# Optimization experiments

Hardware: AMD Instinct MI355X
Metric: run time of the kernel (lower is better)

The kernel has to match this reference:

```python
import jax, jax.numpy as jnp
import numpy as np

N_NODES = 60000
SEQ_LEN = 30
VOCAB = 50000
D_IN = 100     # text_input_size
H = 100        # tweet_embed_size (GRU hidden)
H1 = 100       # hidden_size1
H2 = 100       # hidden_size2
N_EDGES = 120000
N_BATCH = 128


def setup_inputs() -> dict:
    key = jax.random.key(0)
    ks = jax.random.split(key, 16)
    s = 0.05
    return {
        'merged_tree_feature': jax.random.randint(ks[0], (N_NODES, SEQ_LEN), 0, VOCAB, dtype=jnp.int64) if jax.config.jax_enable_x64 else jax.random.randint(ks[0], (N_NODES, SEQ_LEN), 0, VOCAB, dtype=jnp.int32),
        'merged_tree_edge_index': jax.random.randint(ks[1], (2, N_EDGES), 0, N_NODES, dtype=jnp.int32),
        'indices': jax.random.randint(ks[2], (N_NODES,), 0, N_BATCH, dtype=jnp.int32),
        'h0': jax.random.normal(ks[3], (1, N_NODES, H), dtype=jnp.float32),
        'emb': jax.random.normal(ks[4], (VOCAB, D_IN), dtype=jnp.float32) * s,
        'W_ih': jax.random.normal(ks[5], (3 * H, D_IN), dtype=jnp.float32) * s,
        'W_hh': jax.random.normal(ks[6], (3 * H, H), dtype=jnp.float32) * s,
        'b_ih': jnp.zeros((3 * H,), dtype=jnp.float32),
        'b_hh': jnp.zeros((3 * H,), dtype=jnp.float32),
        'W1': jax.random.normal(ks[7], (H, H1), dtype=jnp.float32) * s,
        'b1': jnp.zeros((H1,), dtype=jnp.float32),
        'W2': jax.random.normal(ks[8], (H + H1, H2), dtype=jnp.float32) * s,
        'b2': jnp.zeros((H2,), dtype=jnp.float32),
    }


def _gru(x_seq, h0, W_ih, W_hh, b_ih, b_hh):
    # x_seq: [L, N, D_IN], h0: [N, H]. torch nn.GRU cell math.
    Wx = jnp.einsum('lnd,gd->lng', x_seq, W_ih) + b_ih  # [L, N, 3H]
    Hdim = h0.shape[-1]

    def step(h, wx):
        gh = h @ W_hh.T + b_hh                     # [N, 3H]
        ir, iz, inn = jnp.split(wx, 3, axis=-1)
        hr, hz, hn = jnp.split(gh, 3, axis=-1)
        r = jax.nn.sigmoid(ir + hr)
        z = jax.nn.sigmoid(iz + hz)
        n = jnp.tanh(inn + r * hn)
        h = (1.0 - z) * n + z * h
        return h, None

    hN, _ = jax.lax.scan(step, h0, Wx)
    return hN  # [N, H]


def _gcn_conv(x, W, b, src, dst, n_nodes):
    # PyG GCNConv: self-loops + symmetric normalization.
    xw = x @ W                                                # [N, F]
    ones = jnp.ones(src.shape, dtype=xw.dtype)
    deg = jax.ops.segment_sum(ones, dst, num_segments=n_nodes) + 1.0  # incl. self-loop
    dinv = jax.lax.rsqrt(deg)
    coef = dinv[src] * dinv[dst]                              # [E]
    agg = jax.ops.segment_sum(xw[src] * coef[:, None], dst, num_segments=n_nodes)
    return agg + xw * (dinv * dinv)[:, None] + b


def _forward(merged_tree_feature, merged_tree_edge_index, indices, h0,
             emb, W_ih, W_hh, b_ih, b_hh, W1, b1, W2, b2):
    n = merged_tree_feature.shape[0]
    x_seq = emb[merged_tree_feature]                # [N, L, D_IN]
    x_seq = jnp.transpose(x_seq, (1, 0, 2))         # [L, N, D_IN]
    hn = _gru(x_seq, h0[0], W_ih, W_hh, b_ih, b_hh)  # [N, H]
    src, dst = merged_tree_edge_index[0], merged_tree_edge_index[1]
    x1 = hn
    xc1 = _gcn_conv(x1, W1, b1, src, dst, n)        # [N, H1]
    x2 = xc1
    # root_extend[i] = x1[indices[i]] (loop over batches == gather by batch id)
    root1 = x1[indices]                             # [N, H]
    x = jax.nn.relu(jnp.concatenate([xc1, root1], axis=1))
    # dropout is identity in eval/reference
    xc2 = _gcn_conv(x, W2, b2, src, dst, n)         # [N, H2]
    x = jax.nn.relu(xc2)
    root2 = x2[indices]                             # [N, H1]
    return jnp.concatenate([x, root2], axis=1)      # [N, H2 + H1]


def reference(merged_tree_feature, merged_tree_edge_index, indices, h0,
              emb, W_ih, W_hh, b_ih, b_hh, W1, b1, W2, b2):
    return _forward(merged_tree_feature, merged_tree_edge_index, indices, h0,
                    emb, W_ih, W_hh, b_ih, b_hh, W1, b1, W2, b2)
```

## Files before the change

### kernel.cpp

```cpp
#include <hip/hip_runtime.h>
#include <math.h>

#define D_IN 100
#define H    100
#define SEQL 30

typedef __attribute__((ext_vector_type(8))) short bf16x8;
typedef __attribute__((ext_vector_type(4))) float f32x4;

__device__ __forceinline__ short f2bf(float f) {
    unsigned u = __builtin_bit_cast(unsigned, f);
    unsigned r = (u + 0x7FFFu + ((u >> 16) & 1u)) >> 16;
    return (short)r;
}
__device__ __forceinline__ float bf2f(short s) {
    unsigned u = ((unsigned)(unsigned short)s) << 16;
    return __builtin_bit_cast(float, u);
}

__global__ void k_bpack(const float* __restrict__ W_hh, short* __restrict__ Bhi,
                        short* __restrict__ Blo, int total ) {
    int t = blockIdx.x * blockDim.x + threadIdx.x;
    if (t >= total) return;
    int i    = t & 7;
    int lane = (t >> 3) & 63;
    int blk  = t >> 9;
    int ks = blk & 3, nt = blk >> 2;
    int np = nt * 16 + (lane & 15);
    int k  = ks * 32 + ((lane >> 4) << 3) + i;
    int g = np / 112, j = np % 112;
    float v = (j < 100 && k < 100) ? W_hh[(g * 100 + j) * 100 + k] : 0.f;
    short hi = f2bf(v);
    short lo = f2bf(v - bf2f(hi));
    Bhi[t] = hi;
    Blo[t] = lo;
}

__global__ void k_pack(const float* __restrict__ W, short* __restrict__ Ph,
                       short* __restrict__ Pl, int K, int J, int ld, int trans,
                       int KS, int total) {
    int t = blockIdx.x * blockDim.x + threadIdx.x;
    if (t >= total) return;
    int i    = t & 7;
    int lane = (t >> 3) & 63;
    int blk  = t >> 9;
    int ks = blk % KS, ct = blk / KS;
    int j = ct * 16 + (lane & 15);
    int k = ks * 32 + ((lane >> 4) << 3) + i;
    float v = 0.f;
    if (j < J && k < K) v = trans ? W[(long)j * ld + k] : W[(long)k * ld + j];
    short hi = f2bf(v);
    Ph[t] = hi;
    Pl[t] = f2bf(v - bf2f(hi));
}

template <int KS>
__global__ __launch_bounds__(448) void k_gemm(
        const float* __restrict__ A, int K, int nrows,
        const short* __restrict__ Bh, const short* __restrict__ Bl,
        const float* __restrict__ bias, float* __restrict__ out, int ldo,
        int J, int CT, int ileave) {
    constexpr int Kp  = KS * 32;
    constexpr int STR = Kp + 8;
    __shared__ short sA[2][64 * STR];

    const int tid  = threadIdx.x;
    const int w    = tid >> 6;
    const int lane = tid & 63;
    const int n0   = lane & 15;
    const int q    = lane >> 4;
    const int row0 = blockIdx.x * 64;

    for (int idx = tid; idx < 64 * Kp; idx += 448) {
        int nd = idx / Kp, c = idx % Kp;
        int r = row0 + nd; if (r >= nrows) r = nrows - 1;
        float v = (c < K) ? A[(long)r * K + c] : 0.f;
        short hi = f2bf(v);
        sA[0][nd * STR + c] = hi;
        sA[1][nd * STR + c] = f2bf(v - bf2f(hi));
    }
    __syncthreads();

    for (int ct = w; ct < CT; ct += 7) {
        bf16x8 bh[KS], bl[KS];
#pragma unroll
        for (int ks = 0; ks < KS; ++ks) {
            long bo = ((long)(ct * KS + ks) * 64 + lane) * 8;
            bh[ks] = *(const bf16x8*)&Bh[bo];
            bl[ks] = *(const bf16x8*)&Bl[bo];
        }
        const int j = ct * 16 + n0;
        const bool jv = (j < J);
        const float bv = (bias != nullptr && jv) ? bias[j] : 0.f;
        const long obase = ileave ? ((long)(j % 100) * 3 + (j / 100)) : (long)j;

#pragma unroll
        for (int t = 0; t < 4; ++t) {
            f32x4 acc = (f32x4){0.f, 0.f, 0.f, 0.f};
#pragma unroll
            for (int ks = 0; ks < KS; ++ks) {
                int off = (t * 16 + n0) * STR + ks * 32 + q * 8;
                bf16x8 aHi = *(const bf16x8*)&sA[0][off];
                bf16x8 aLo = *(const bf16x8*)&sA[1][off];
                acc = __builtin_amdgcn_mfma_f32_16x16x32_bf16(aHi, bh[ks], acc, 0, 0, 0);
                acc = __builtin_amdgcn_mfma_f32_16x16x32_bf16(aHi, bl[ks], acc, 0, 0, 0);
                acc = __builtin_amdgcn_mfma_f32_16x16x32_bf16(aLo, bh[ks], acc, 0, 0, 0);
            }
            if (jv) {
#pragma unroll
                for (int r = 0; r < 4; ++r) {
                    int row = row0 + t * 16 + 4 * q + r;
                    if (row < nrows) out[(long)row * ldo + obase] = acc[r] + bv;
                }
            }
        }
    }
}

__global__ __launch_bounds__(448) void k_gemm_cat(
        const float* __restrict__ xc1, const float* __restrict__ hn,
        const int* __restrict__ idx, int nrows,
        const short* __restrict__ Bh, const short* __restrict__ Bl,
        float* __restrict__ out, int CT) {
    constexpr int KS = 7, Kp = 224, STR = 232;
    __shared__ short sA[2][64 * STR];

    const int tid  = threadIdx.x;
    const int w    = tid >> 6;
    const int lane = tid & 63;
    const int n0   = lane & 15;
    const int q    = lane >> 4;
    const int row0 = blockIdx.x * 64;

    for (int t = tid; t < 64 * Kp; t += 448) {
        int nd = t / Kp, c = t % Kp;
        int r = row0 + nd; if (r >= nrows) r = nrows - 1;
        float v = 0.f;
        if (c < 100)      v = fmaxf(xc1[(long)r * 100 + c], 0.f);
        else if (c < 200) v = fmaxf(hn[(long)idx[r] * 100 + (c - 100)], 0.f);
        short hi = f2bf(v);
        sA[0][nd * STR + c] = hi;
        sA[1][nd * STR + c] = f2bf(v - bf2f(hi));
    }
    __syncthreads();

    for (int ct = w; ct < CT; ct += 7) {
        bf16x8 bh[KS], bl[KS];
#pragma unroll
        for (int ks = 0; ks < KS; ++ks) {
            long bo = ((long)(ct * KS + ks) * 64 + lane) * 8;
            bh[ks] = *(const bf16x8*)&Bh[bo];
            bl[ks] = *(const bf16x8*)&Bl[bo];
        }
        const int j = ct * 16 + n0;
        const bool jv = (j < 100);

#pragma unroll
        for (int t4 = 0; t4 < 4; ++t4) {
            f32x4 acc = (f32x4){0.f, 0.f, 0.f, 0.f};
#pragma unroll
            for (int ks = 0; ks < KS; ++ks) {
                int off = (t4 * 16 + n0) * STR + ks * 32 + q * 8;
                bf16x8 aHi = *(const bf16x8*)&sA[0][off];
                bf16x8 aLo = *(const bf16x8*)&sA[1][off];
                acc = __builtin_amdgcn_mfma_f32_16x16x32_bf16(aHi, bh[ks], acc, 0, 0, 0);
                acc = __builtin_amdgcn_mfma_f32_16x16x32_bf16(aHi, bl[ks], acc, 0, 0, 0);
                acc = __builtin_amdgcn_mfma_f32_16x16x32_bf16(aLo, bh[ks], acc, 0, 0, 0);
            }
            if (jv) {
#pragma unroll
                for (int r = 0; r < 4; ++r) {
                    int row = row0 + t4 * 16 + 4 * q + r;
                    if (row < nrows) out[(long)row * 100 + j] = acc[r];
                }
            }
        }
    }
}

__global__ __launch_bounds__(448, 2) void k_gru_mfma(
        const int* __restrict__ tok, const float* __restrict__ h0,
        const float* __restrict__ Wemb, const short* __restrict__ Bhi,
        const short* __restrict__ Blo, const float* __restrict__ b_hh,
        float* __restrict__ hout, int n_nodes) {
    __shared__ short hA[2][2][48 * 136];

    const int tid  = threadIdx.x;
    const int w    = tid >> 6;
    const int lane = tid & 63;
    const int n0   = lane & 15;
    const int q    = lane >> 4;
    const int node0 = blockIdx.x * 48;

    bf16x8 bh[3][4], bl[3][4];
#pragma unroll
    for (int g = 0; g < 3; ++g)
#pragma unroll
        for (int ks = 0; ks < 4; ++ks) {
            long bo = ((long)((g * 7 + w) * 4 + ks) * 64 + lane) * 8;
            bh[g][ks] = *(const bf16x8*)&Bhi[bo];
            bl[g][ks] = *(const bf16x8*)&Blo[bo];
        }

    for (int i = tid; i < 48 * 128; i += 448) {
        int nd = i >> 7, c = i & 127;
        int row = node0 + nd; if (row >= n_nodes) row = n_nodes - 1;
        float v = (c < 100) ? h0[(long)row * 100 + c] : 0.f;
        short hi = f2bf(v);
        hA[0][0][nd * 136 + c] = hi;
        hA[0][1][nd * 136 + c] = f2bf(v - bf2f(hi));
        hA[1][0][nd * 136 + c] = 0;
        hA[1][1][nd * 136 + c] = 0;
    }

    const int j   = 16 * w + n0;
    const int jc  = j < 100 ? j : 99;
    const bool jok = (j < 100);
    const float bhr = b_hh[jc], bhz = b_hh[100 + jc], bhn = b_hh[200 + jc];

    int rows0[4], rows1[4], rows2[4];
#pragma unroll
    for (int r = 0; r < 4; ++r) {
        int a0 = node0 + 4 * q + r;
        int a1 = a0 + 16;
        int a2 = a0 + 32;
        rows0[r] = a0 < n_nodes ? a0 : n_nodes - 1;
        rows1[r] = a1 < n_nodes ? a1 : n_nodes - 1;
        rows2[r] = a2 < n_nodes ? a2 : n_nodes - 1;
    }
    float hp0[4], hp1[4], hp2[4];
#pragma unroll
    for (int r = 0; r < 4; ++r) hp0[r] = h0[(long)rows0[r] * 100 + jc];
#pragma unroll
    for (int r = 0; r < 4; ++r) hp1[r] = h0[(long)rows1[r] * 100 + jc];
#pragma unroll
    for (int r = 0; r < 4; ++r) hp2[r] = h0[(long)rows2[r] * 100 + jc];

    __syncthreads();

    int tb0[4], tb1[4], tb2[4];
#pragma unroll
    for (int r = 0; r < 4; ++r) tb0[r] = tok[(long)rows0[r] * SEQL] * 300;
#pragma unroll
    for (int r = 0; r < 4; ++r) tb1[r] = tok[(long)rows1[r] * SEQL] * 300;
#pragma unroll
    for (int r = 0; r < 4; ++r) tb2[r] = tok[(long)rows2[r] * SEQL] * 300;

    const int jc3 = 3 * jc;

    int cur = 0;
#pragma unroll 1
    for (int l = 0; l < SEQL; ++l) {
        float wxA[12], wxB[12];
#pragma unroll
        for (int r = 0; r < 4; ++r) {
            const float* p = Wemb + (long)tb0[r] + jc3;
            wxA[r] = p[0]; wxA[4 + r] = p[1]; wxA[8 + r] = p[2];
        }
#pragma unroll
        for (int r = 0; r < 4; ++r) {
            const float* p = Wemb + (long)tb1[r] + jc3;
            wxB[r] = p[0]; wxB[4 + r] = p[1]; wxB[8 + r] = p[2];
        }

        int tnx[4], tny[4], tnz[4];
        if (l < SEQL - 1) {
#pragma unroll
            for (int r = 0; r < 4; ++r) tnx[r] = tok[(long)rows0[r] * SEQL + l + 1] * 300;
#pragma unroll
            for (int r = 0; r < 4; ++r) tny[r] = tok[(long)rows1[r] * SEQL + l + 1] * 300;
#pragma unroll
            for (int r = 0; r < 4; ++r) tnz[r] = tok[(long)rows2[r] * SEQL + l + 1] * 300;
        }

        const short* hc0 = &hA[cur][0][0];
        const short* hc1 = &hA[cur][1][0];
        short* hn0 = &hA[cur ^ 1][0][0];
        short* hn1 = &hA[cur ^ 1][1][0];

        f32x4 acc[3];
        auto epi = [&](const float* wx, float* hp, int ndo) {
#pragma unroll
            for (int r = 0; r < 4; ++r) {
                float pr = wx[r]     + acc[0][r] + bhr;
                float pz = wx[4 + r] + acc[1][r] + bhz;
                float rr = __builtin_amdgcn_rcpf(1.f + __expf(-pr));
                float zz = __builtin_amdgcn_rcpf(1.f + __expf(-pz));
                float pn = wx[8 + r] + rr * (acc[2][r] + bhn);
                float th = 1.f - 2.f * __builtin_amdgcn_rcpf(1.f + __expf(2.f * pn));
                float hnew = (1.f - zz) * th + zz * hp[r];
                hp[r] = hnew;
                if (jok) {
                    int off = (ndo + 4 * q + r) * 136 + j;
                    short hi = f2bf(hnew);
                    hn0[off] = hi;
                    hn1[off] = f2bf(hnew - bf2f(hi));
                }
            }
        };

        {
            bf16x8 aHi[4], aLo[4];
#pragma unroll
            for (int ks = 0; ks < 4; ++ks) {
                int off = n0 * 136 + ks * 32 + q * 8;
                aHi[ks] = *(const bf16x8*)&hc0[off];
                aLo[ks] = *(const bf16x8*)&hc1[off];
            }
#pragma unroll
            for (int g = 0; g < 3; ++g) acc[g] = (f32x4){0.f, 0.f, 0.f, 0.f};
#pragma unroll
            for (int g = 0; g < 3; ++g)
#pragma unroll
                for (int ks = 0; ks < 4; ++ks) {
                    acc[g] = __builtin_amdgcn_mfma_f32_16x16x32_bf16(aHi[ks], bh[g][ks], acc[g], 0, 0, 0);
                    acc[g] = __builtin_amdgcn_mfma_f32_16x16x32_bf16(aHi[ks], bl[g][ks], acc[g], 0, 0, 0);
                    acc[g] = __builtin_amdgcn_mfma_f32_16x16x32_bf16(aLo[ks], bh[g][ks], acc[g], 0, 0, 0);
                }
            epi(wxA, hp0, 0);
        }

        float wxC[12];
#pragma unroll
        for (int r = 0; r < 4; ++r) {
            const float* p = Wemb + (long)tb2[r] + jc3;
            wxC[r] = p[0]; wxC[4 + r] = p[1]; wxC[8 + r] = p[2];
        }

        {
            bf16x8 aHi[4], aLo[4];
#pragma unroll
            for (int ks = 0; ks < 4; ++ks) {
                int off = (16 + n0) * 136 + ks * 32 + q * 8;
                aHi[ks] = *(const bf16x8*)&hc0[off];
                aLo[ks] = *(const bf16x8*)&hc1[off];
            }
#pragma unroll
            for (int g = 0; g < 3; ++g) acc[g] = (f32x4){0.f, 0.f, 0.f, 0.f};
#pragma unroll
            for (int g = 0; g < 3; ++g)
#pragma unroll
                for (int ks = 0; ks < 4; ++ks) {
                    acc[g] = __builtin_amdgcn_mfma_f32_16x16x32_bf16(aHi[ks], bh[g][ks], acc[g], 0, 0, 0);
                    acc[g] = __builtin_amdgcn_mfma_f32_16x16x32_bf16(aHi[ks], bl[g][ks], acc[g], 0, 0, 0);
                    acc[g] = __builtin_amdgcn_mfma_f32_16x16x32_bf16(aLo[ks], bh[g][ks], acc[g], 0, 0, 0);
                }
            epi(wxB, hp1, 16);
        }

        {
            bf16x8 aHi[4], aLo[4];
#pragma unroll
            for (int ks = 0; ks < 4; ++ks) {
                int off = (32 + n0) * 136 + ks * 32 + q * 8;
                aHi[ks] = *(const bf16x8*)&hc0[off];
                aLo[ks] = *(const bf16x8*)&hc1[off];
            }
#pragma unroll
            for (int g = 0; g < 3; ++g) acc[g] = (f32x4){0.f, 0.f, 0.f, 0.f};
#pragma unroll
            for (int g = 0; g < 3; ++g)
#pragma unroll
                for (int ks = 0; ks < 4; ++ks) {
                    acc[g] = __builtin_amdgcn_mfma_f32_16x16x32_bf16(aHi[ks], bh[g][ks], acc[g], 0, 0, 0);
                    acc[g] = __builtin_amdgcn_mfma_f32_16x16x32_bf16(aHi[ks], bl[g][ks], acc[g], 0, 0, 0);
                    acc[g] = __builtin_amdgcn_mfma_f32_16x16x32_bf16(aLo[ks], bh[g][ks], acc[g], 0, 0, 0);
                }
            epi(wxC, hp2, 32);
        }

        if (l < SEQL - 1) {
#pragma unroll
            for (int r = 0; r < 4; ++r) { tb0[r] = tnx[r]; tb1[r] = tny[r]; tb2[r] = tnz[r]; }
        }
        __syncthreads();
        cur ^= 1;
    }

    for (int i = tid; i < 48 * 100; i += 448) {
        int nd = i / 100, c = i % 100;
        if (node0 + nd < n_nodes)
            hout[(long)(node0 + nd) * 100 + c] =
                bf2f(hA[cur][0][nd * 136 + c]) + bf2f(hA[cur][1][nd * 136 + c]);
    }
}

__global__ void k_deg(const int* __restrict__ dst, int* __restrict__ degi, int E) {
    int e = blockIdx.x * blockDim.x + threadIdx.x;
    if (e < E) atomicAdd(&degi[dst[e]], 1);
}

__global__ __launch_bounds__(256) void k_scan_bsum(const int* __restrict__ degi,
                                                   int* __restrict__ bsum, int N) {
    __shared__ int sh[256];
    int t = threadIdx.x, i = blockIdx.x * 256 + t;
    sh[t] = (i < N) ? degi[i] : 0;
    __syncthreads();
    for (int o = 128; o > 0; o >>= 1) {
        if (t < o) sh[t] += sh[t + o];
        __syncthreads();
    }
    if (t == 0) bsum[blockIdx.x] = sh[0];
}

__global__ __launch_bounds__(1024) void k_scan_part(int* __restrict__ bsum, int G) {
    __shared__ int sh[1024];
    int t = threadIdx.x;
    int v = (t < G) ? bsum[t] : 0;
    sh[t] = v;
    __syncthreads();
    for (int o = 1; o < 1024; o <<= 1) {
        int a = (t >= o) ? sh[t - o] : 0;
        __syncthreads();
        sh[t] += a;
        __syncthreads();
    }
    if (t < G) bsum[t] = sh[t] - v;
}

__global__ __launch_bounds__(256) void k_scan_emit(const int* __restrict__ degi,
                                                   const int* __restrict__ bsum,
                                                   int* __restrict__ rs, int* __restrict__ cursor,
                                                   float* __restrict__ dinv, int N, int E) {
    __shared__ int sh[256];
    int t = threadIdx.x, i = blockIdx.x * 256 + t;
    int d = (i < N) ? degi[i] : 0;
    sh[t] = d;
    __syncthreads();
    for (int o = 1; o < 256; o <<= 1) {
        int a = (t >= o) ? sh[t - o] : 0;
        __syncthreads();
        sh[t] += a;
        __syncthreads();
    }
    if (i < N) {
        int run = bsum[blockIdx.x] + sh[t] - d;
        rs[i] = run;
        cursor[i] = run;
        dinv[i] = rsqrtf((float)d + 1.0f);
        if (i == N - 1) rs[N] = E;
    }
}

__global__ void k_scatter(const int* __restrict__ src, const int* __restrict__ dst,
                          int* __restrict__ cursor, int* __restrict__ esrc, int E) {
    int e = blockIdx.x * blockDim.x + threadIdx.x;
    if (e >= E) return;
    int pos = atomicAdd(&cursor[dst[e]], 1);
    esrc[pos] = src[e];
}

__global__ void k_conv1_fin(const int* __restrict__ rs, const int* __restrict__ esrc,
                            const float* __restrict__ xw, const float* __restrict__ dinv,
                            const float* __restrict__ b1, float* __restrict__ xc1, int N) {
    int t = blockIdx.x * blockDim.x + threadIdx.x;
    if (t >= N * 25) return;
    int n = t / 25, jq = t % 25;
    float dn = dinv[n];
    float4 acc = {0.f, 0.f, 0.f, 0.f};
    int e1 = rs[n + 1];
    for (int e = rs[n]; e < e1; ++e) {
        int s = esrc[e];
        float ds = dinv[s];
        float4 xs = ((const float4*)xw)[s * 25 + jq];
        acc.x = fmaf(xs.x, ds, acc.x);
        acc.y = fmaf(xs.y, ds, acc.y);
        acc.z = fmaf(xs.z, ds, acc.z);
        acc.w = fmaf(xs.w, ds, acc.w);
    }
    float4 xs = ((const float4*)xw)[t];
    float4 bq = ((const float4*)b1)[jq];
    float dn2 = dn * dn;
    float4 v;
    v.x = fmaf(acc.x, dn, fmaf(xs.x, dn2, bq.x));
    v.y = fmaf(acc.y, dn, fmaf(xs.y, dn2, bq.y));
    v.z = fmaf(acc.z, dn, fmaf(xs.z, dn2, bq.z));
    v.w = fmaf(acc.w, dn, fmaf(xs.w, dn2, bq.w));
    ((float4*)xc1)[t] = v;
}

__global__ void k_conv2_fin(const int* __restrict__ rs, const int* __restrict__ esrc,
                            const float* __restrict__ xw, const float* __restrict__ dinv,
                            const float* __restrict__ b2, const float* __restrict__ xc1,
                            const int* __restrict__ idx, float* __restrict__ out, int N) {
    int t = blockIdx.x * blockDim.x + threadIdx.x;
    if (t >= N * 25) return;
    int n = t / 25, jq = t % 25;
    float dn = dinv[n];
    float4 acc = {0.f, 0.f, 0.f, 0.f};
    int e1 = rs[n + 1];
    for (int e = rs[n]; e < e1; ++e) {
        int s = esrc[e];
        float ds = dinv[s];
        float4 xs = ((const float4*)xw)[s * 25 + jq];
        acc.x = fmaf(xs.x, ds, acc.x);
        acc.y = fmaf(xs.y, ds, acc.y);
        acc.z = fmaf(xs.z, ds, acc.z);
        acc.w = fmaf(xs.w, ds, acc.w);
    }
    float4 xs = ((const float4*)xw)[t];
    float4 bq = ((const float4*)b2)[jq];
    float dn2 = dn * dn;
    float4 v;
    v.x = fmaxf(fmaf(acc.x, dn, fmaf(xs.x, dn2, bq.x)), 0.f);
    v.y = fmaxf(fmaf(acc.y, dn, fmaf(xs.y, dn2, bq.y)), 0.f);
    v.z = fmaxf(fmaf(acc.z, dn, fmaf(xs.z, dn2, bq.z)), 0.f);
    v.w = fmaxf(fmaf(acc.w, dn, fmaf(xs.w, dn2, bq.w)), 0.f);
    float4 rv = ((const float4*)xc1)[(long)idx[n] * 25 + jq];
    ((float4*)out)[n * 50 + jq] = v;
    ((float4*)out)[n * 50 + 25 + jq] = rv;
}

extern "C" void kernel_launch(void* const* d_in, const int* in_sizes, int n_in,
                              void* d_out, int out_size, void* d_ws, size_t ws_size,
                              hipStream_t stream) {
    const int*   feat    = (const int*)d_in[0];
    const int*   edges   = (const int*)d_in[1];
    const int*   indices = (const int*)d_in[2];
    const float* h0      = (const float*)d_in[3];
    const float* emb     = (const float*)d_in[4];
    const float* W_ih    = (const float*)d_in[5];
    const float* W_hh    = (const float*)d_in[6];
    const float* b_ih    = (const float*)d_in[7];
    const float* b_hh    = (const float*)d_in[8];
    const float* W1      = (const float*)d_in[9];
    const float* b1      = (const float*)d_in[10];
    const float* W2      = (const float*)d_in[11];
    const float* b2      = (const float*)d_in[12];
    float* out = (float*)d_out;

    const int N = in_sizes[2];
    const int E = in_sizes[1] / 2;
    const int V = in_sizes[4] / D_IN;
    const int* src = edges;
    const int* dst = edges + E;

    float* ws   = (float*)d_ws;
    float* hbuf = ws;
    float* Wemb = hbuf + (long)N * H;
    float* xw   = Wemb;
    float* xc1  = Wemb + (long)V * 300;
    float* xbig = xc1 + (long)N * 100;
    float* dinv = xbig + (long)N * 200;
    short* Bhi  = (short*)(dinv + N);
    short* Blo  = Bhi + 43008;
    short* PihH = Blo + 43008;
    short* PihL = PihH + 38912;
    short* P1H  = PihL + 38912;
    short* P1L  = P1H + 14336;
    short* P2H  = P1L + 14336;
    short* P2L  = P2H + 25088;
    int*   degi = (int*)(P2L + 25088);
    int*   rs   = degi + N;
    int*   cursor = rs + N + 1;
    int*   esrc = cursor + N;
    int*   bsum = esrc + E;
    (void)ws_size; (void)n_in; (void)out_size;

    const int B = 256;
    const int Gs = (N + 255) / 256;

    hipMemsetAsync(degi, 0, (size_t)N * sizeof(int), stream);
    k_deg<<<(E + B - 1) / B, B, 0, stream>>>(dst, degi, E);
    k_scan_bsum<<<Gs, 256, 0, stream>>>(degi, bsum, N);
    k_scan_part<<<1, 1024, 0, stream>>>(bsum, Gs);
    k_scan_emit<<<Gs, 256, 0, stream>>>(degi, bsum, rs, cursor, dinv, N, E);
    k_scatter<<<(E + B - 1) / B, B, 0, stream>>>(src, dst, cursor, esrc, E);

    k_bpack<<<(43008 + B - 1) / B, B, 0, stream>>>(W_hh, Bhi, Blo, 43008);
    k_pack<<<(38912 + B - 1) / B, B, 0, stream>>>(W_ih, PihH, PihL, 100, 300, 100, 1, 4, 38912);
    k_pack<<<(14336 + B - 1) / B, B, 0, stream>>>(W1, P1H, P1L, 100, 100, 100, 0, 4, 14336);
    k_pack<<<(25088 + B - 1) / B, B, 0, stream>>>(W2, P2H, P2L, 200, 100, 100, 0, 7, 25088);

    k_gemm<4><<<(V + 63) / 64, 448, 0, stream>>>(emb, 100, V, PihH, PihL, b_ih,
                                                 Wemb, 300, 300, 19, 1);

    k_gru_mfma<<<(N + 47) / 48, 448, 0, stream>>>(feat, h0, Wemb, Bhi, Blo, b_hh, hbuf, N);

    {
        k_gemm<4><<<(N + 63) / 64, 448, 0, stream>>>(hbuf, 100, N, P1H, P1L, nullptr,
                                                     xw, 100, 100, 7, 0);
        int nquads = N * 25;
        k_conv1_fin<<<(nquads + B - 1) / B, B, 0, stream>>>(rs, esrc, xw, dinv, b1, xc1, N);
        k_gemm_cat<<<(N + 63) / 64, 448, 0, stream>>>(xc1, hbuf, indices, N,
                                                      P2H, P2L, xw, 7);
        k_conv2_fin<<<(nquads + B - 1) / B, B, 0, stream>>>(rs, esrc, xw, dinv, b2, xc1,
                                                            indices, out, N);
    }
}
```

Before: 1.000 ms.

## Merge weight-pack kernels, vectorize GEMM staging, reorder GRU MFMA tiles

Combines the four weight-packing launches into one kernel, which cuts launch overhead. The GEMM and concat-GEMM shared-memory staging loops now load float4 and write 4-wide bf16 hi/lo pairs instead of scalars. The GRU step issues all Wemb gathers up front and interleaves the three MFMA tiles with the epilogues, so MFMA work can overlap the elementwise math. This adds register pressure from three live accumulator sets. The float4 loads also assume row strides that are multiples of 4.

Result: slower. 1.083 ms (+8.2%).

```diff
diff --git a/kernel.cpp b/kernel.cpp
--- a/kernel.cpp
+++ b/kernel.cpp
@@ -6,6 +6,7 @@
 #define SEQL 30
 
 typedef __attribute__((ext_vector_type(8))) short bf16x8;
+typedef __attribute__((ext_vector_type(4))) short s16x4;
 typedef __attribute__((ext_vector_type(4))) float f32x4;
 
 __device__ __forceinline__ short f2bf(float f) {
@@ -18,10 +19,9 @@
     return __builtin_bit_cast(float, u);
 }
 
-__global__ void k_bpack(const float* __restrict__ W_hh, short* __restrict__ Bhi,
-                        short* __restrict__ Blo, int total ) {
-    int t = blockIdx.x * blockDim.x + threadIdx.x;
-    if (t >= total) return;
+__device__ __forceinline__ void bpack_one(const float* __restrict__ W_hh,
+                                          short* __restrict__ Bhi,
+                                          short* __restrict__ Blo, int t) {
     int i    = t & 7;
     int lane = (t >> 3) & 63;
     int blk  = t >> 9;
@@ -31,16 +31,13 @@
     int g = np / 112, j = np % 112;
     float v = (j < 100 && k < 100) ? W_hh[(g * 100 + j) * 100 + k] : 0.f;
     short hi = f2bf(v);
-    short lo = f2bf(v - bf2f(hi));
     Bhi[t] = hi;
-    Blo[t] = lo;
-}
-
-__global__ void k_pack(const float* __restrict__ W, short* __restrict__ Ph,
-                       short* __restrict__ Pl, int K, int J, int ld, int trans,
-                       int KS, int total) {
-    int t = blockIdx.x * blockDim.x + threadIdx.x;
-    if (t >= total) return;
+    Blo[t] = f2bf(v - bf2f(hi));
+}
+
+__device__ __forceinline__ void pack_one(const float* __restrict__ W,
+                                         short* __restrict__ Ph, short* __restrict__ Pl,
+                                         int K, int J, int ld, int trans, int KS, int t) {
     int i    = t & 7;
     int lane = (t >> 3) & 63;
     int blk  = t >> 9;
@@ -54,6 +51,22 @@
     Pl[t] = f2bf(v - bf2f(hi));
 }
 
+__global__ void k_packall(const float* __restrict__ W_hh, const float* __restrict__ W_ih,
+                          const float* __restrict__ W1, const float* __restrict__ W2,
+                          short* __restrict__ Bhi, short* __restrict__ Blo,
+                          short* __restrict__ PihH, short* __restrict__ PihL,
+                          short* __restrict__ P1H, short* __restrict__ P1L,
+                          short* __restrict__ P2H, short* __restrict__ P2L) {
+    int t = blockIdx.x * blockDim.x + threadIdx.x;
+    if (t < 43008) { bpack_one(W_hh, Bhi, Blo, t); return; }
+    t -= 43008;
+    if (t < 38912) { pack_one(W_ih, PihH, PihL, 100, 300, 100, 1, 4, t); return; }
+    t -= 38912;
+    if (t < 14336) { pack_one(W1, P1H, P1L, 100, 100, 100, 0, 4, t); return; }
+    t -= 14336;
+    if (t < 25088) { pack_one(W2, P2H, P2L, 200, 100, 100, 0, 7, t); return; }
+}
+
 template <int KS>
 __global__ __launch_bounds__(448) void k_gemm(
         const float* __restrict__ A, int K, int nrows,
@@ -61,6 +74,7 @@
         const float* __restrict__ bias, float* __restrict__ out, int ldo,
         int J, int CT, int ileave) {
     constexpr int Kp  = KS * 32;
+    constexpr int C4  = Kp / 4;
     constexpr int STR = Kp + 8;
     __shared__ short sA[2][64 * STR];
 
@@ -71,13 +85,19 @@
     const int q    = lane >> 4;
     const int row0 = blockIdx.x * 64;
 
-    for (int idx = tid; idx < 64 * Kp; idx += 448) {
-        int nd = idx / Kp, c = idx % Kp;
+    const int K4 = K / 4;
+    for (int idx = tid; idx < 64 * C4; idx += 448) {
+        int nd = idx / C4, c4 = idx % C4;
         int r = row0 + nd; if (r >= nrows) r = nrows - 1;
-        float v = (c < K) ? A[(long)r * K + c] : 0.f;
-        short hi = f2bf(v);
-        sA[0][nd * STR + c] = hi;
-        sA[1][nd * STR + c] = f2bf(v - bf2f(hi));
+        float4 v = {0.f, 0.f, 0.f, 0.f};
+        if (c4 < K4) v = *(const float4*)&A[(long)r * K + 4 * c4];
+        s16x4 hi, lo;
+        hi.x = f2bf(v.x); lo.x = f2bf(v.x - bf2f(hi.x));
+        hi.y = f2bf(v.y); lo.y = f2bf(v.y - bf2f(hi.y));
+        hi.z = f2bf(v.z); lo.z = f2bf(v.z - bf2f(hi.z));
+        hi.w = f2bf(v.w); lo.w = f2bf(v.w - bf2f(hi.w));
+        *(s16x4*)&sA[0][nd * STR + 4 * c4] = hi;
+        *(s16x4*)&sA[1][nd * STR + 4 * c4] = lo;
     }
     __syncthreads();
 
@@ -122,7 +142,7 @@
         const int* __restrict__ idx, int nrows,
         const short* __restrict__ Bh, const short* __restrict__ Bl,
         float* __restrict__ out, int CT) {
-    constexpr int KS = 7, Kp = 224, STR = 232;
+    constexpr int KS = 7, Kp = 224, STR = 232, C4 = 56;
     __shared__ short sA[2][64 * STR];
 
     const int tid  = threadIdx.x;
@@ -132,15 +152,21 @@
     const int q    = lane >> 4;
     const int row0 = blockIdx.x * 64;
 
-    for (int t = tid; t < 64 * Kp; t += 448) {
-        int nd = t / Kp, c = t % Kp;
+    for (int t = tid; t < 64 * C4; t += 448) {
+        int nd = t / C4, c4 = t % C4;
         int r = row0 + nd; if (r >= nrows) r = nrows - 1;
-        float v = 0.f;
-        if (c < 100)      v = fmaxf(xc1[(long)r * 100 + c], 0.f);
-        else if (c < 200) v = fmaxf(hn[(long)idx[r] * 100 + (c - 100)], 0.f);
-        short hi = f2bf(v);
-        sA[0][nd * STR + c] = hi;
-        sA[1][nd * STR + c] = f2bf(v - bf2f(hi));
+        float4 v = {0.f, 0.f, 0.f, 0.f};
+        if (c4 < 25)      v = *(const float4*)&xc1[(long)r * 100 + 4 * c4];
+        else if (c4 < 50) v = *(const float4*)&hn[(long)idx[r] * 100 + 4 * (c4 - 25)];
+        v.x = fmaxf(v.x, 0.f); v.y = fmaxf(v.y, 0.f);
+        v.z = fmaxf(v.z, 0.f); v.w = fmaxf(v.w, 0.f);
+        s16x4 hi, lo;
+        hi.x = f2bf(v.x); lo.x = f2bf(v.x - bf2f(hi.x));
+        hi.y = f2bf(v.y); lo.y = f2bf(v.y - bf2f(hi.y));
+        hi.z = f2bf(v.z); lo.z = f2bf(v.z - bf2f(hi.z));
+        hi.w = f2bf(v.w); lo.w = f2bf(v.w - bf2f(hi.w));
+        *(s16x4*)&sA[0][nd * STR + 4 * c4] = hi;
+        *(s16x4*)&sA[1][nd * STR + 4 * c4] = lo;
     }
     __syncthreads();
 
@@ -218,40 +244,38 @@
     const bool jok = (j < 100);
     const float bhr = b_hh[jc], bhz = b_hh[100 + jc], bhn = b_hh[200 + jc];
 
-    int rows0[4], rows1[4], rows2[4];
+    long rl0[4], rl1[4], rl2[4];
+    float hp0[4], hp1[4], hp2[4];
 #pragma unroll
     for (int r = 0; r < 4; ++r) {
         int a0 = node0 + 4 * q + r;
         int a1 = a0 + 16;
         int a2 = a0 + 32;
-        rows0[r] = a0 < n_nodes ? a0 : n_nodes - 1;
-        rows1[r] = a1 < n_nodes ? a1 : n_nodes - 1;
-        rows2[r] = a2 < n_nodes ? a2 : n_nodes - 1;
-    }
-    float hp0[4], hp1[4], hp2[4];
-#pragma unroll
-    for (int r = 0; r < 4; ++r) hp0[r] = h0[(long)rows0[r] * 100 + jc];
-#pragma unroll
-    for (int r = 0; r < 4; ++r) hp1[r] = h0[(long)rows1[r] * 100 + jc];
-#pragma unroll
-    for (int r = 0; r < 4; ++r) hp2[r] = h0[(long)rows2[r] * 100 + jc];
+        a0 = a0 < n_nodes ? a0 : n_nodes - 1;
+        a1 = a1 < n_nodes ? a1 : n_nodes - 1;
+        a2 = a2 < n_nodes ? a2 : n_nodes - 1;
+        rl0[r] = (long)a0 * SEQL; rl1[r] = (long)a1 * SEQL; rl2[r] = (long)a2 * SEQL;
+        hp0[r] = h0[(long)a0 * 100 + jc];
+        hp1[r] = h0[(long)a1 * 100 + jc];
+        hp2[r] = h0[(long)a2 * 100 + jc];
+    }
 
     __syncthreads();
 
     int tb0[4], tb1[4], tb2[4];
 #pragma unroll
-    for (int r = 0; r < 4; ++r) tb0[r] = tok[(long)rows0[r] * SEQL] * 300;
-#pragma unroll
-    for (int r = 0; r < 4; ++r) tb1[r] = tok[(long)rows1[r] * SEQL] * 300;
-#pragma unroll
-    for (int r = 0; r < 4; ++r) tb2[r] = tok[(long)rows2[r] * SEQL] * 300;
+    for (int r = 0; r < 4; ++r) tb0[r] = tok[rl0[r]] * 300;
+#pragma unroll
+    for (int r = 0; r < 4; ++r) tb1[r] = tok[rl1[r]] * 300;
+#pragma unroll
+    for (int r = 0; r < 4; ++r) tb2[r] = tok[rl2[r]] * 300;
 
     const int jc3 = 3 * jc;
 
     int cur = 0;
 #pragma unroll 1
     for (int l = 0; l < SEQL; ++l) {
-        float wxA[12], wxB[12];
+        float wxA[12], wxB[12], wxC[12];
 #pragma unroll
         for (int r = 0; r < 4; ++r) {
             const float* p = Wemb + (long)tb0[r] + jc3;
@@ -262,15 +286,19 @@
             const float* p = Wemb + (long)tb1[r] + jc3;
             wxB[r] = p[0]; wxB[4 + r] = p[1]; wxB[8 + r] = p[2];
         }
-
+#pragma unroll
+        for (int r = 0; r < 4; ++r) {
+            const float* p = Wemb + (long)tb2[r] + jc3;
+            wxC[r] = p[0]; wxC[4 + r] = p[1]; wxC[8 + r] = p[2];
+        }
         int tnx[4], tny[4], tnz[4];
         if (l < SEQL - 1) {
 #pragma unroll
-            for (int r = 0; r < 4; ++r) tnx[r] = tok[(long)rows0[r] * SEQL + l + 1] * 300;
-#pragma unroll
-            for (int r = 0; r < 4; ++r) tny[r] = tok[(long)rows1[r] * SEQL + l + 1] * 300;
-#pragma unroll
-            for (int r = 0; r < 4; ++r) tnz[r] = tok[(long)rows2[r] * SEQL + l + 1] * 300;
+            for (int r = 0; r < 4; ++r) tnx[r] = tok[rl0[r] + l + 1] * 300;
+#pragma unroll
+            for (int r = 0; r < 4; ++r) tny[r] = tok[rl1[r] + l + 1] * 300;
+#pragma unroll
+            for (int r = 0; r < 4; ++r) tnz[r] = tok[rl2[r] + l + 1] * 300;
         }
 
         const short* hc0 = &hA[cur][0][0];
@@ -278,8 +306,7 @@
         short* hn0 = &hA[cur ^ 1][0][0];
         short* hn1 = &hA[cur ^ 1][1][0];
 
-        f32x4 acc[3];
-        auto epi = [&](const float* wx, float* hp, int ndo) {
+        auto epi = [&](const float* wx, float* hp, int ndo, const f32x4* acc) {
 #pragma unroll
             for (int r = 0; r < 4; ++r) {
                 float pr = wx[r]     + acc[0][r] + bhr;
@@ -298,12 +325,11 @@
                 }
             }
         };
-
-        {
+        auto mfma_tile = [&](int ndo, f32x4* acc) {
             bf16x8 aHi[4], aLo[4];
 #pragma unroll
             for (int ks = 0; ks < 4; ++ks) {
-                int off = n0 * 136 + ks * 32 + q * 8;
+                int off = (ndo + n0) * 136 + ks * 32 + q * 8;
                 aHi[ks] = *(const bf16x8*)&hc0[off];
                 aLo[ks] = *(const bf16x8*)&hc1[off];
             }
@@ -317,57 +343,15 @@
                     acc[g] = __builtin_amdgcn_mfma_f32_16x16x32_bf16(aHi[ks], bl[g][ks], acc[g], 0, 0, 0);
                     acc[g] = __builtin_amdgcn_mfma_f32_16x16x32_bf16(aLo[ks], bh[g][ks], acc[g], 0, 0, 0);
                 }
-            epi(wxA, hp0, 0);
-        }
-
-        float wxC[12];
-#pragma unroll
-        for (int r = 0; r < 4; ++r) {
-            const float* p = Wemb + (long)tb2[r] + jc3;
-            wxC[r] = p[0]; wxC[4 + r] = p[1]; wxC[8 + r] = p[2];
-        }
-
-        {
-            bf16x8 aHi[4], aLo[4];
-#pragma unroll
-            for (int ks = 0; ks < 4; ++ks) {
-                int off = (16 + n0) * 136 + ks * 32 + q * 8;
-                aHi[ks] = *(const bf16x8*)&hc0[off];
-                aLo[ks] = *(const bf16x8*)&hc1[off];
-            }
-#pragma unroll
-            for (int g = 0; g < 3; ++g) acc[g] = (f32x4){0.f, 0.f, 0.f, 0.f};
-#pragma unroll
-            for (int g = 0; g < 3; ++g)
-#pragma unroll
-                for (int ks = 0; ks < 4; ++ks) {
-                    acc[g] = __builtin_amdgcn_mfma_f32_16x16x32_bf16(aHi[ks], bh[g][ks], acc[g], 0, 0, 0);
-                    acc[g] = __builtin_amdgcn_mfma_f32_16x16x32_bf16(aHi[ks], bl[g][ks], acc[g], 0, 0, 0);
-                    acc[g] = __builtin_amdgcn_mfma_f32_16x16x32_bf16(aLo[ks], bh[g][ks], acc[g], 0, 0, 0);
-                }
-            epi(wxB, hp1, 16);
-        }
-
-        {
-            bf16x8 aHi[4], aLo[4];
-#pragma unroll
-            for (int ks = 0; ks < 4; ++ks) {
-                int off = (32 + n0) * 136 + ks * 32 + q * 8;
-                aHi[ks] = *(const bf16x8*)&hc0[off];
-                aLo[ks] = *(const bf16x8*)&hc1[off];
-            }
-#pragma unroll
-            for (int g = 0; g < 3; ++g) acc[g] = (f32x4){0.f, 0.f, 0.f, 0.f};
-#pragma unroll
-            for (int g = 0; g < 3; ++g)
-#pragma unroll
-                for (int ks = 0; ks < 4; ++ks) {
-                    acc[g] = __builtin_amdgcn_mfma_f32_16x16x32_bf16(aHi[ks], bh[g][ks], acc[g], 0, 0, 0);
-                    acc[g] = __builtin_amdgcn_mfma_f32_16x16x32_bf16(aHi[ks], bl[g][ks], acc[g], 0, 0, 0);
-                    acc[g] = __builtin_amdgcn_mfma_f32_16x16x32_bf16(aLo[ks], bh[g][ks], acc[g], 0, 0, 0);
-                }
-            epi(wxC, hp2, 32);
-        }
+        };
+
+        f32x4 acc0[3], acc1[3], acc2[3];
+        mfma_tile(0, acc0);
+        mfma_tile(16, acc1);
+        epi(wxA, hp0, 0, acc0);
+        mfma_tile(32, acc2);
+        epi(wxB, hp1, 16, acc1);
+        epi(wxC, hp2, 32, acc2);
 
         if (l < SEQL - 1) {
 #pragma unroll
@@ -567,10 +551,9 @@
     k_scan_emit<<<Gs, 256, 0, stream>>>(degi, bsum, rs, cursor, dinv, N, E);
     k_scatter<<<(E + B - 1) / B, B, 0, stream>>>(src, dst, cursor, esrc, E);
 
-    k_bpack<<<(43008 + B - 1) / B, B, 0, stream>>>(W_hh, Bhi, Blo, 43008);
-    k_pack<<<(38912 + B - 1) / B, B, 0, stream>>>(W_ih, PihH, PihL, 100, 300, 100, 1, 4, 38912);
-    k_pack<<<(14336 + B - 1) / B, B, 0, stream>>>(W1, P1H, P1L, 100, 100, 100, 0, 4, 14336);
-    k_pack<<<(25088 + B - 1) / B, B, 0, stream>>>(W2, P2H, P2L, 200, 100, 100, 0, 7, 25088);
+    k_packall<<<(121344 + B - 1) / B, B, 0, stream>>>(W_hh, W_ih, W1, W2,
+                                                      Bhi, Blo, PihH, PihL,
+                                                      P1H, P1L, P2H, P2L);
 
     k_gemm<4><<<(V + 63) / 64, 448, 0, stream>>>(emb, 100, V, PihH, PihL, b_ih,
                                                  Wemb, 300, 300, 19, 1);
```
